# Kernel optimization log

Hardware: AMD Instinct MI355X
Metric: run time of the kernel (lower is better)

Reference implementation:

```python
import jax, jax.numpy as jnp
import numpy as np

B, N, S, D, H = 4, 64, 512, 128, 8  # batch, groups, set size, in_size, heads


def setup_inputs() -> dict:
    key = jax.random.key(0)
    ks = jax.random.split(key, 8)
    s1 = 1.0 / np.sqrt(D)
    s2 = 1.0 / np.sqrt(2 * D)
    return {
        "x": jax.random.normal(ks[0], (B, N, S, D), jnp.float32),
        # DeepSets phi MLP: D -> D -> D -> D (hidden=[in_size,in_size])
        "w1": jax.random.normal(ks[1], (D, D), jnp.float32) * s1,
        "b1": jnp.zeros((D,), jnp.float32),
        "w2": jax.random.normal(ks[2], (D, D), jnp.float32) * s1,
        "b2": jnp.zeros((D,), jnp.float32),
        "w3": jax.random.normal(ks[3], (D, D), jnp.float32) * s1,
        "b3": jnp.zeros((D,), jnp.float32),
        # attention projection: 2D -> H*D
        "W": jax.random.normal(ks[4], (2 * D, H * D), jnp.float32) * s2,
        "Wb": jnp.zeros((H * D,), jnp.float32),
        # per-head query vector (zeros-init in original; random for a nontrivial baseline)
        "q": jax.random.normal(ks[5], (H, D), jnp.float32) * 0.1,
    }


def reference(x, w1, b1, w2, b2, w3, b3, W, Wb, q):
    # SetTransform (DeepSets): per-element MLP then sum over set dim (-2)
    h = jax.nn.relu(x @ w1 + b1)
    h = jax.nn.relu(h @ w2 + b2)
    h = h @ w3 + b3
    set_feat = h.sum(axis=-2)                                  # (B, N, D)
    sf = jnp.broadcast_to(set_feat[..., None, :], x.shape)      # (B, N, S, D)
    comb = jnp.concatenate([x, sf], axis=-1)                    # (B, N, S, 2D)
    heads = (comb @ W + Wb).reshape(B, N, S, H, D)              # (B, N, S, H, D)
    e = jnp.einsum('bnshd,hd->bnsh', heads, q)                  # (B, N, S, H)
    return jax.nn.softmax(e, axis=-2)                           # softmax over set dim
```

## Files before the change

kernel.cpp:

```cpp
#include <hip/hip_runtime.h>

#define Bsz 4
#define Ngrp 64
#define Sset 512
#define Din 128
#define Hh 8
#define EST (Sset + 1)

#define DPP_QUAD_XOR1 0xB1
#define DPP_QUAD_XOR2 0x4E
#define DPP_ROW_HALF_MIRROR 0x141
#define DPP_ROW_MIRROR 0x140

template <int CTRL>
__device__ __forceinline__ float dpp_add(float v) {
    int perm = __builtin_amdgcn_update_dpp(0, __float_as_int(v), CTRL, 0xF, 0xF, true);
    return v + __int_as_float(perm);
}

__device__ __forceinline__ float row16_sum(float v) {
    v = dpp_add<DPP_QUAD_XOR1>(v);
    v = dpp_add<DPP_QUAD_XOR2>(v);
    v = dpp_add<DPP_ROW_HALF_MIRROR>(v);
    v = dpp_add<DPP_ROW_MIRROR>(v);
    return v;
}

__global__ void __launch_bounds__(256) compute_u_kernel(
    const float* __restrict__ W,
    const float* __restrict__ q,
    float* __restrict__ u)
{
    const int tid = threadIdx.x;
    const int grp = tid >> 4;
    const int sub = tid & 15;

    const int idx = blockIdx.x * 16 + grp;
    const int h = idx >> 7;
    const int c = idx & 127;

    const float4* Wr = (const float4*)(W + (size_t)c * (Hh * Din) + (size_t)h * Din);
    const float4* qr = (const float4*)(q + h * Din);
    const float4 w0 = Wr[sub];
    const float4 w1 = Wr[sub + 16];
    const float4 q0 = qr[sub];
    const float4 q1 = qr[sub + 16];

    float v;
    v = w0.x * q0.x;
    v = fmaf(w0.y, q0.y, v);
    v = fmaf(w0.z, q0.z, v);
    v = fmaf(w0.w, q0.w, v);
    v = fmaf(w1.x, q1.x, v);
    v = fmaf(w1.y, q1.y, v);
    v = fmaf(w1.z, q1.z, v);
    v = fmaf(w1.w, q1.w, v);
    v = row16_sum(v);
    if (sub == 0) u[idx] = v;
}

__global__ void __launch_bounds__(Sset) attn_softmax_kernel(
    const float* __restrict__ x,
    const float* __restrict__ u,
    float* __restrict__ out)
{
    const int bn = blockIdx.x;
    const int tid = threadIdx.x;
    const int wave = tid >> 6;
    const int lane = tid & 63;
    const int g    = lane >> 4;
    const int sub  = lane & 15;

    __shared__ float e_s[Hh * EST];

    const float4* u4 = (const float4*)u;
    float4 ua[Hh], ub[Hh];
#pragma unroll
    for (int h = 0; h < Hh; ++h) {
        ua[h] = u4[h * 32 + sub];
        ub[h] = u4[h * 32 + sub + 16];
    }

    const float4* xb = (const float4*)(x + (size_t)bn * Sset * Din);
#pragma unroll 4
    for (int pass = 0; pass < 16; ++pass) {
        const int r = wave * 64 + pass * 4 + g;
        const float4* xr = xb + (size_t)r * (Din / 4);
        const float4 x0 = xr[sub];
        const float4 x1 = xr[sub + 16];

        float st = 0.f;
#pragma unroll
        for (int h = 0; h < Hh; ++h) {
            float v;
            v = x0.x * ua[h].x;
            v = fmaf(x0.y, ua[h].y, v);
            v = fmaf(x0.z, ua[h].z, v);
            v = fmaf(x0.w, ua[h].w, v);
            v = fmaf(x1.x, ub[h].x, v);
            v = fmaf(x1.y, ub[h].y, v);
            v = fmaf(x1.z, ub[h].z, v);
            v = fmaf(x1.w, ub[h].w, v);
            v = row16_sum(v);
            if (sub == h) st = v;
        }
        if (sub < Hh) e_s[sub * EST + r] = st;
    }
    __syncthreads();

    {
        float* eh = &e_s[wave * EST];

        float m = -1e30f;
#pragma unroll
        for (int k = 0; k < Sset / 64; ++k) m = fmaxf(m, eh[lane + 64 * k]);
#pragma unroll
        for (int off = 32; off >= 1; off >>= 1) m = fmaxf(m, __shfl_xor(m, off, 64));

        float p[Sset / 64];
        float sum = 0.f;
#pragma unroll
        for (int k = 0; k < Sset / 64; ++k) {
            p[k] = __expf(eh[lane + 64 * k] - m);
            sum += p[k];
        }
#pragma unroll
        for (int off = 32; off >= 1; off >>= 1) sum += __shfl_xor(sum, off, 64);

        const float inv = 1.f / sum;
#pragma unroll
        for (int k = 0; k < Sset / 64; ++k) eh[lane + 64 * k] = p[k] * inv;
    }
    __syncthreads();

    {
        const int s = tid;
        float4 o0, o1;
        o0.x = e_s[0 * EST + s];
        o0.y = e_s[1 * EST + s];
        o0.z = e_s[2 * EST + s];
        o0.w = e_s[3 * EST + s];
        o1.x = e_s[4 * EST + s];
        o1.y = e_s[5 * EST + s];
        o1.z = e_s[6 * EST + s];
        o1.w = e_s[7 * EST + s];
        float4* orow = (float4*)(out + ((size_t)bn * Sset + s) * Hh);
        orow[0] = o0;
        orow[1] = o1;
    }
}

extern "C" void kernel_launch(void* const* d_in, const int* in_sizes, int n_in,
                              void* d_out, int out_size, void* d_ws, size_t ws_size,
                              hipStream_t stream) {
    const float* x = (const float*)d_in[0];
    const float* W = (const float*)d_in[7];
    const float* q = (const float*)d_in[9];
    float* u = (float*)d_ws;
    float* out = (float*)d_out;

    compute_u_kernel<<<dim3(64), dim3(256), 0, stream>>>(W, q, u);
    attn_softmax_kernel<<<dim3(Bsz * Ngrp), dim3(Sset), 0, stream>>>(x, u, out);
}
```

Before: 118.0 us.

## Double threads per block and software-prefetch x rows across passes

The attention kernel moves to 1024 threads per block, so each wave handles 32 rows instead of 64. The row loop is fully unrolled and prefetches x two passes ahead in registers, with the first loads issued before the u loads. Only the first eight waves do the softmax, and the output store is split into one float4 per thread. The goal is more memory-level parallelism to hide global-load latency, at the cost of higher register pressure and idle waves during the softmax.

```diff
diff --git a/kernel.cpp b/kernel.cpp
--- a/kernel.cpp
+++ b/kernel.cpp
@@ -59,7 +59,7 @@
     if (sub == 0) u[idx] = v;
 }
 
-__global__ void __launch_bounds__(Sset) attn_softmax_kernel(
+__global__ void __launch_bounds__(1024) attn_softmax_kernel(
     const float* __restrict__ x,
     const float* __restrict__ u,
     float* __restrict__ out)
@@ -71,7 +71,15 @@
     const int g    = lane >> 4;
     const int sub  = lane & 15;
 
-    __shared__ float e_s[Hh * EST];
+    __shared__ __align__(16) float e_s[Hh * EST];
+
+    const float4* xb = (const float4*)(x + (size_t)bn * Sset * Din);
+
+    const int rbase = wave * 32 + g;
+    float4 cx0 = xb[(size_t)(rbase + 0) * 32 + sub];
+    float4 cx1 = xb[(size_t)(rbase + 0) * 32 + sub + 16];
+    float4 nx0 = xb[(size_t)(rbase + 4) * 32 + sub];
+    float4 nx1 = xb[(size_t)(rbase + 4) * 32 + sub + 16];
 
     const float4* u4 = (const float4*)u;
     float4 ua[Hh], ub[Hh];
@@ -81,13 +89,16 @@
         ub[h] = u4[h * 32 + sub + 16];
     }
 
-    const float4* xb = (const float4*)(x + (size_t)bn * Sset * Din);
-#pragma unroll 4
-    for (int pass = 0; pass < 16; ++pass) {
-        const int r = wave * 64 + pass * 4 + g;
-        const float4* xr = xb + (size_t)r * (Din / 4);
-        const float4 x0 = xr[sub];
-        const float4 x1 = xr[sub + 16];
+#pragma unroll
+    for (int pass = 0; pass < 8; ++pass) {
+        const float4 x0 = cx0, x1 = cx1;
+        cx0 = nx0; cx1 = nx1;
+        if (pass < 6) {
+            const int rn = rbase + (pass + 2) * 4;
+            nx0 = xb[(size_t)rn * 32 + sub];
+            nx1 = xb[(size_t)rn * 32 + sub + 16];
+        }
+        const int r = rbase + pass * 4;
 
         float st = 0.f;
 #pragma unroll
@@ -108,7 +119,7 @@
     }
     __syncthreads();
 
-    {
+    if (wave < Hh) {
         float* eh = &e_s[wave * EST];
 
         float m = -1e30f;
@@ -134,19 +145,14 @@
     __syncthreads();
 
     {
-        const int s = tid;
-        float4 o0, o1;
-        o0.x = e_s[0 * EST + s];
-        o0.y = e_s[1 * EST + s];
-        o0.z = e_s[2 * EST + s];
-        o0.w = e_s[3 * EST + s];
-        o1.x = e_s[4 * EST + s];
-        o1.y = e_s[5 * EST + s];
-        o1.z = e_s[6 * EST + s];
-        o1.w = e_s[7 * EST + s];
-        float4* orow = (float4*)(out + ((size_t)bn * Sset + s) * Hh);
-        orow[0] = o0;
-        orow[1] = o1;
+        const int s = tid >> 1;
+        const int half = tid & 1;
+        float4 o;
+        o.x = e_s[(half * 4 + 0) * EST + s];
+        o.y = e_s[(half * 4 + 1) * EST + s];
+        o.z = e_s[(half * 4 + 2) * EST + s];
+        o.w = e_s[(half * 4 + 3) * EST + s];
+        ((float4*)(out + ((size_t)bn * Sset + s) * Hh))[half] = o;
     }
 }
 
@@ -160,5 +166,5 @@
     float* out = (float*)d_out;
 
     compute_u_kernel<<<dim3(64), dim3(256), 0, stream>>>(W, q, u);
-    attn_softmax_kernel<<<dim3(Bsz * Ngrp), dim3(Sset), 0, stream>>>(x, u, out);
+    attn_softmax_kernel<<<dim3(Bsz * Ngrp), dim3(1024), 0, stream>>>(x, u, out);
 }
```

After: 113.4 us. -3.9%, faster.
